# Kernel optimization log

Hardware: AMD Instinct MI355X
Metric: run time of the kernel (lower is better)

The kernel has to match this reference:

```python
import jax, jax.numpy as jnp
import numpy as np

B, L, E, H = 2, 2048, 1024, 16
D = E // H  # head dim = 64


def setup_inputs() -> dict:
    key = jax.random.key(0)
    ks = jax.random.split(key, 10)
    s = 0.02
    return {
        "xt": jax.random.normal(ks[0], (B, L, E), jnp.float32),
        "xs": jax.random.normal(ks[1], (B, L, E), jnp.float32),
        "Wt": jax.random.normal(ks[2], (E, 3 * E), jnp.float32) * s,  # t_attn weight (x @ Wt)
        "bt": jnp.zeros((3 * E,), jnp.float32),
        "Ws": jax.random.normal(ks[3], (E, 2 * E), jnp.float32) * s,  # s_attn weight
        "bs": jnp.zeros((2 * E,), jnp.float32),
        "Wc": jax.random.normal(ks[4], (E, E), jnp.float32) * s,      # c_proj weight
        "bc": jnp.zeros((E,), jnp.float32),
        "lam_ts": jnp.ones((1,), jnp.float32),
        "lam_st": jnp.ones((1,), jnp.float32),
        "lam_ss": jnp.ones((1,), jnp.float32),
    }


def _heads(x):
    # (B, L, E) -> (B, H, L, D)
    return x.reshape(B, L, H, D).transpose(0, 2, 1, 3)


def reference(xt, xs, Wt, bt, Ws, bs, Wc, bc, lam_ts, lam_st, lam_ss):
    qt, kt, vt = jnp.split(xt @ Wt + bt, 3, axis=2)
    qs, ks = jnp.split(xs @ Ws + bs, 2, axis=2)
    qt, kt, vt, qs, ks = map(_heads, (qt, kt, vt, qs, ks))

    # 4-way disentangled scores; fuse the 4 matmuls into 2 by combining keys:
    # qt@kt^T + lam_ts*qt@ks^T = qt @ (kt + lam_ts*ks)^T
    # lam_st*qs@kt^T + lam_ss*qs@ks^T = qs @ (lam_st*kt + lam_ss*ks)^T
    k1 = kt + lam_ts[0] * ks
    k2 = lam_st[0] * kt + lam_ss[0] * ks
    att = (jnp.einsum('bhqd,bhkd->bhqk', qt, k1)
           + jnp.einsum('bhqd,bhkd->bhqk', qs, k2)) * (1.0 / np.sqrt(D))
    att = jax.nn.softmax(att, axis=-1)
    y = jnp.einsum('bhqk,bhkd->bhqd', att, vt)  # (B, H, L, D)
    y = y.transpose(0, 2, 1, 3).reshape(B, L, E)
    return y @ Wc + bc
```

## Files before the change

kernel.cpp:

```cpp
#include <hip/hip_runtime.h>
#include <math.h>

#define LQ 2048
#define EQ 1024
#define M_ROWS 4096
#define BH 32

typedef _Float16 f16x8 __attribute__((ext_vector_type(8)));
typedef _Float16 f16x4 __attribute__((ext_vector_type(4)));
typedef _Float16 f16x2 __attribute__((ext_vector_type(2)));
typedef float f32x4 __attribute__((ext_vector_type(4)));
typedef float f32x16 __attribute__((ext_vector_type(16)));

#define QSCALE 0.1803368801111204f
#define DEFER_THR 8.0f

__device__ __forceinline__ void async_ld16(const _Float16* g, _Float16* l) {
  __builtin_amdgcn_global_load_lds(
      (const __attribute__((address_space(1))) unsigned int*)g,
      (__attribute__((address_space(3))) unsigned int*)l, 16, 0, 0);
}

__global__ __launch_bounds__(256) void prep(
    const float* __restrict__ xt, const float* __restrict__ xs,
    const float* __restrict__ Wt, const float* __restrict__ Ws,
    const float* __restrict__ Wc,
    _Float16* __restrict__ xt16, _Float16* __restrict__ xs16,
    _Float16* __restrict__ WtT, _Float16* __restrict__ WsT,
    _Float16* __restrict__ WcT) {
  int gb = blockIdx.x;
  if (gb < 4096) {
    int i = gb * 256 + threadIdx.x;
    const float* s; _Float16* d; size_t off;
    if (i < 524288) { s = xt; d = xt16; off = (size_t)i * 8; }
    else            { s = xs; d = xs16; off = (size_t)(i - 524288) * 8; }
    float4 a = *(const float4*)&s[off];
    float4 b = *(const float4*)&s[off + 4];
    f16x8 h;
    h[0] = (_Float16)a.x; h[1] = (_Float16)a.y; h[2] = (_Float16)a.z; h[3] = (_Float16)a.w;
    h[4] = (_Float16)b.x; h[5] = (_Float16)b.y; h[6] = (_Float16)b.z; h[7] = (_Float16)b.w;
    *(f16x8*)&d[off] = h;
  } else {
    __shared__ float T[32][65];
    int tb = gb - 4096;
    int c0 = (tb % 96) * 64;
    int k0 = (tb / 96) * 32;
    const float* W; _Float16* D; int Nw, cl;
    if (c0 < 3072)      { W = Wt; D = WtT; Nw = 3072; cl = c0; }
    else if (c0 < 5120) { W = Ws; D = WsT; Nw = 2048; cl = c0 - 3072; }
    else                { W = Wc; D = WcT; Nw = 1024; cl = c0 - 5120; }
    const int tid = threadIdx.x;
#pragma unroll
    for (int p = 0; p < 4; ++p) {
      int idx = tid + p * 256;
      int row = idx >> 5;
      int c2 = (idx & 31) * 2;
      float2 v = *(const float2*)&W[(size_t)(k0 + row) * Nw + cl + c2];
      T[row][c2] = v.x;
      T[row][c2 + 1] = v.y;
    }
    __syncthreads();
#pragma unroll
    for (int p = 0; p < 4; ++p) {
      int idx = tid + p * 256;
      int col = idx >> 4;
      int k2 = (idx & 15) * 2;
      f16x2 h2;
      h2[0] = (_Float16)T[k2][col];
      h2[1] = (_Float16)T[k2 + 1][col];
      *(f16x2*)&D[(size_t)(cl + col) * 1024 + k0 + k2] = h2;
    }
  }
}

__global__ __launch_bounds__(256, 3) void proj_gemm(
    const _Float16* __restrict__ xt16, const _Float16* __restrict__ xs16,
    const _Float16* __restrict__ WtT, const _Float16* __restrict__ WsT,
    const float* __restrict__ bt, const float* __restrict__ bs,
    _Float16* __restrict__ q16, _Float16* __restrict__ k16,
    _Float16* __restrict__ v16) {
  __shared__ _Float16 Al[128 * 64];
  __shared__ _Float16 Bl[128 * 64];

  const int tid = threadIdx.x;
  const int w = tid >> 6;
  const int lane = tid & 63;
  const int quad = lane >> 4;
  const int l15 = lane & 15;
  const int wm = w >> 1, wn = w & 1;
  const int by = blockIdx.y;
  const int n0 = blockIdx.x * 128;

  const _Float16* Ab;
  const _Float16* Bb;
  const float* bias;
  int m0, bsel = 0, branch;
  if (by < 32) {
    branch = 0; Ab = xt16; Bb = WtT; bias = bt; m0 = by * 128;
  } else if (by < 48) {
    branch = 1;
    int by2 = by - 32;
    bsel = by2 >> 3;
    m0 = (by2 & 7) * 128;
    Ab = WtT + (size_t)2048 * 1024;
    Bb = xt16 + (size_t)bsel * 2048 * 1024;
    bias = bt;
  } else {
    branch = 2; Ab = xs16; Bb = WsT; bias = bs; m0 = (by - 48) * 128;
  }

  const int srow = lane >> 3;
  const int sch = lane & 7;

  f32x4 acc[4][4];
#pragma unroll
  for (int mb = 0; mb < 4; ++mb)
#pragma unroll
    for (int nb = 0; nb < 4; ++nb) acc[mb][nb] = (f32x4){0.f, 0.f, 0.f, 0.f};

  for (int kt = 0; kt < 1024; kt += 64) {
    __syncthreads();
#pragma unroll
    for (int a = 0; a < 4; ++a) {
      int row = w * 32 + a * 8 + srow;
      int sc = sch ^ (row & 7);
      async_ld16(&Ab[(size_t)(m0 + row) * 1024 + kt + sc * 8], &Al[(w * 32 + a * 8) * 64]);
      async_ld16(&Bb[(size_t)(n0 + row) * 1024 + kt + sc * 8], &Bl[(w * 32 + a * 8) * 64]);
    }
    __syncthreads();

#pragma unroll
    for (int g = 0; g < 2; ++g) {
      f16x8 af[4], bf[4];
#pragma unroll
      for (int mb = 0; mb < 4; ++mb) {
        int row = wm * 64 + mb * 16 + l15;
        int pc = ((g * 4 + quad) ^ (row & 7)) * 8;
        af[mb] = *(const f16x8*)&Al[row * 64 + pc];
      }
#pragma unroll
      for (int nb = 0; nb < 4; ++nb) {
        int row = wn * 64 + nb * 16 + l15;
        int pc = ((g * 4 + quad) ^ (row & 7)) * 8;
        bf[nb] = *(const f16x8*)&Bl[row * 64 + pc];
      }
#pragma unroll
      for (int mb = 0; mb < 4; ++mb)
#pragma unroll
        for (int nb = 0; nb < 4; ++nb)
          acc[mb][nb] = __builtin_amdgcn_mfma_f32_16x16x32_f16(af[mb], bf[nb], acc[mb][nb], 0, 0, 0);
    }
  }

#pragma unroll
  for (int mb = 0; mb < 4; ++mb)
#pragma unroll
    for (int nb = 0; nb < 4; ++nb)
#pragma unroll
      for (int r = 0; r < 4; ++r) {
        int row = m0 + wm * 64 + mb * 16 + quad * 4 + r;
        int col = n0 + wn * 64 + nb * 16 + l15;
        if (branch == 1) {
          float val = acc[mb][nb][r] + bias[2048 + row];
          v16[(size_t)(bsel * 1024 + row) * 2048 + col] = (_Float16)val;
        } else {
          float val = acc[mb][nb][r] + bias[col];
          int bb = row >> 11, ll = row & 2047;
          int which = col >> 10, e = col & 1023;
          int hh = e >> 6, dd = e & 63;
          size_t rowhd = (size_t)(bb * 16 + hh) * 2048 + ll;
          int off = (branch == 0) ? 0 : 64;
          if (which == 0) q16[rowhd * 128 + off + dd] = (_Float16)val;
          else            k16[rowhd * 128 + off + dd] = (_Float16)val;
        }
      }
}

__global__ __launch_bounds__(256, 3) void cproj_gemm(
    const _Float16* __restrict__ A, const _Float16* __restrict__ Bm,
    const float* __restrict__ bias, float* __restrict__ outf) {
  __shared__ _Float16 Al0[128 * 32];
  __shared__ _Float16 Bl0[64 * 32];
  __shared__ _Float16 Al1[128 * 32];
  __shared__ _Float16 Bl1[64 * 32];

  const int tid = threadIdx.x;
  const int w = tid >> 6;
  const int lane = tid & 63;
  const int quad = lane >> 4;
  const int l15 = lane & 15;
  const int wm = w >> 1, wn = w & 1;
  const int m0 = blockIdx.y * 128;
  const int n0 = blockIdx.x * 64;

  const int srow = lane >> 2;
  const int schunk = ((lane & 3) ^ ((lane >> 3) & 3)) * 8;

  f32x4 acc[4][2];
#pragma unroll
  for (int mb = 0; mb < 4; ++mb)
#pragma unroll
    for (int nb = 0; nb < 2; ++nb) acc[mb][nb] = (f32x4){0.f, 0.f, 0.f, 0.f};

  const int key = (l15 >> 1) & 3;

  auto dma = [&](int kt, _Float16* Al, _Float16* Bl) {
#pragma unroll
    for (int i = 0; i < 2; ++i) {
      int rt = w * 32 + i * 16;
      async_ld16(&A[(size_t)(m0 + rt + srow) * 1024 + kt + schunk], &Al[rt * 32]);
    }
    int rtb = w * 16;
    async_ld16(&Bm[(size_t)(n0 + rtb + srow) * 1024 + kt + schunk], &Bl[rtb * 32]);
  };

  auto comp = [&](const _Float16* Al, const _Float16* Bl) {
    f16x8 af[4], bf[2];
    const int pc = (quad ^ key) * 8;
#pragma unroll
    for (int mb = 0; mb < 4; ++mb)
      af[mb] = *(const f16x8*)&Al[(wm * 64 + mb * 16 + l15) * 32 + pc];
#pragma unroll
    for (int nb = 0; nb < 2; ++nb)
      bf[nb] = *(const f16x8*)&Bl[(wn * 32 + nb * 16 + l15) * 32 + pc];
#pragma unroll
    for (int mb = 0; mb < 4; ++mb)
#pragma unroll
      for (int nb = 0; nb < 2; ++nb)
        acc[mb][nb] = __builtin_amdgcn_mfma_f32_16x16x32_f16(af[mb], bf[nb], acc[mb][nb], 0, 0, 0);
  };

  dma(0, Al0, Bl0);
  for (int kt = 0; kt < 1024; kt += 64) {
    __syncthreads();
    dma(kt + 32, Al1, Bl1);
    comp(Al0, Bl0);
    __syncthreads();
    if (kt + 64 < 1024) dma(kt + 64, Al0, Bl0);
    comp(Al1, Bl1);
  }

#pragma unroll
  for (int mb = 0; mb < 4; ++mb)
#pragma unroll
    for (int nb = 0; nb < 2; ++nb)
#pragma unroll
      for (int r = 0; r < 4; ++r) {
        int row = m0 + wm * 64 + mb * 16 + quad * 4 + r;
        int col = n0 + wn * 32 + nb * 16 + l15;
        outf[(size_t)row * 1024 + col] = acc[mb][nb][r] + bias[col];
      }
}

__global__ __launch_bounds__(256, 2) void flash_attn_mfma(
    const _Float16* __restrict__ qcat, const _Float16* __restrict__ kcat,
    const _Float16* __restrict__ vT, _Float16* __restrict__ y,
    const float* __restrict__ lam_ts, const float* __restrict__ lam_st,
    const float* __restrict__ lam_ss) {
  const int bh = blockIdx.y;
  const int qt0 = blockIdx.x * 128;
  const int b = bh >> 4, h = bh & 15;
  const _Float16* Qg = qcat + (size_t)bh * LQ * 128;
  const _Float16* Kg = kcat + (size_t)bh * LQ * 128;
  const _Float16* Vg = vT + (size_t)bh * 64 * LQ;

  __shared__ _Float16 Ksh0[64 * 128];
  __shared__ _Float16 Ksh1[64 * 128];
  __shared__ _Float16 Vsh0[64 * 64];
  __shared__ _Float16 Vsh1[64 * 64];
  __shared__ _Float16 Vsh2[64 * 64];
  __shared__ _Float16 Vsh3[64 * 64];

  const int tid = threadIdx.x;
  const int w = tid >> 6;
  const int lane = tid & 63;
  const int half = lane >> 5;
  const int l31 = lane & 31;

  const float lts = lam_ts[0], lst = lam_st[0], lss = lam_ss[0];

  f16x8 qf[8];
#pragma unroll
  for (int db = 0; db < 4; ++db) {
    const _Float16* qp = &Qg[(size_t)(qt0 + w * 32 + l31) * 128 + db * 16 + half * 8];
    f16x8 a = *(const f16x8*)qp;
    f16x8 bq = *(const f16x8*)(qp + 64);
#pragma unroll
    for (int e = 0; e < 8; ++e) {
      float fa = (float)a[e], fb = (float)bq[e];
      qf[db][e]     = (_Float16)(QSCALE * (fa + lst * fb));
      qf[db + 4][e] = (_Float16)(QSCALE * (lts * fa + lss * fb));
    }
  }

  float m_i = -INFINITY;
  float l_i = 0.f;
  f32x16 O[2];
#pragma unroll
  for (int nt = 0; nt < 2; ++nt)
#pragma unroll
    for (int r = 0; r < 16; ++r) O[nt][r] = 0.f;

  auto dma_k = [&](int t, _Float16* Kd) {
#pragma unroll
    for (int a = 0; a < 4; ++a) {
      int row = w * 16 + a * 4 + (lane >> 4);
      int sc = (lane & 15) ^ (row & 7);
      async_ld16(&Kg[(size_t)(t + row) * 128 + sc * 8], &Kd[(w * 16 + a * 4) * 128]);
    }
  };
  auto dma_v = [&](int t, _Float16* Vd) {
#pragma unroll
    for (int a = 0; a < 2; ++a) {
      int row = w * 16 + a * 8 + (lane >> 3);
      int sc = (lane & 7) ^ (row & 7);
      async_ld16(&Vg[(size_t)row * LQ + t + sc * 8], &Vd[(w * 16 + a * 8) * 64]);
    }
  };

  auto qk = [&](const _Float16* Ks, f32x16* Sp) {
    __builtin_amdgcn_s_setprio(1);
#pragma unroll
    for (int db = 0; db < 8; ++db) {
      const int pc = ((db * 2 + half) ^ (lane & 7)) * 8;
      f16x8 af0 = *(const f16x8*)&Ks[(l31) * 128 + pc];
      f16x8 af1 = *(const f16x8*)&Ks[(32 + l31) * 128 + pc];
      Sp[0] = __builtin_amdgcn_mfma_f32_32x32x16_f16(af0, qf[db], Sp[0], 0, 0, 0);
      Sp[1] = __builtin_amdgcn_mfma_f32_32x32x16_f16(af1, qf[db], Sp[1], 0, 0, 0);
    }
    __builtin_amdgcn_s_setprio(0);
  };

  auto softpv = [&](f32x16* S, const _Float16* Vs0, const _Float16* Vs1) {
    float mx = -INFINITY;
#pragma unroll
    for (int kb = 0; kb < 4; ++kb)
#pragma unroll
      for (int r = 0; r < 16; ++r) mx = fmaxf(mx, S[kb][r]);
    mx = fmaxf(mx, __shfl_xor(mx, 32));

    if (__any(mx > m_i + DEFER_THR)) {
      float m_new = fmaxf(m_i, mx);
      float alpha = __builtin_amdgcn_exp2f(m_i - m_new);
      l_i *= alpha;
#pragma unroll
      for (int nt = 0; nt < 2; ++nt)
#pragma unroll
        for (int r = 0; r < 16; ++r) O[nt][r] *= alpha;
      m_i = m_new;
    }

    float s = 0.f;
#pragma unroll
    for (int kb = 0; kb < 4; ++kb)
#pragma unroll
      for (int r = 0; r < 16; ++r) {
        float p = __builtin_amdgcn_exp2f(S[kb][r] - m_i);
        S[kb][r] = p;
        s += p;
      }
    s += __shfl_xor(s, 32);
    l_i += s;

#pragma unroll
    for (int kb = 0; kb < 4; ++kb) {
      unsigned pu[8];
#pragma unroll
      for (int i = 0; i < 8; ++i) {
        f16x2 t2;
        t2[0] = (_Float16)S[kb][2 * i];
        t2[1] = (_Float16)S[kb][2 * i + 1];
        pu[i] = __builtin_bit_cast(unsigned, t2);
      }
#pragma unroll
      for (int c = 0; c < 2; ++c) {
        unsigned u0 = pu[4 * c + 0], u1 = pu[4 * c + 1];
        unsigned u2 = pu[4 * c + 2], u3 = pu[4 * c + 3];
        asm("v_permlane32_swap_b32 %0, %1" : "+v"(u0), "+v"(u2));
        asm("v_permlane32_swap_b32 %0, %1" : "+v"(u1), "+v"(u3));
        union { unsigned u[4]; f16x8 v; } pb;
        pb.u[0] = u0; pb.u[1] = u1; pb.u[2] = u2; pb.u[3] = u3;
        const int kb2 = kb * 2 + c;
        const _Float16* Vs = (kb2 < 4) ? Vs0 : Vs1;
        const int kb2r = kb2 & 3;
        f16x8 av[2];
#pragma unroll
        for (int nt = 0; nt < 2; ++nt) {
          int dim = nt * 32 + l31;
          int pc = ((kb2r * 2 + half) ^ (dim & 7)) * 8;
          av[nt] = *(const f16x8*)&Vs[dim * 64 + pc];
        }
        __builtin_amdgcn_s_setprio(1);
#pragma unroll
        for (int nt = 0; nt < 2; ++nt)
          O[nt] = __builtin_amdgcn_mfma_f32_32x32x16_f16(av[nt], pb.v, O[nt], 0, 0, 0);
        __builtin_amdgcn_s_setprio(0);
      }
    }
  };

  auto step = [&](int t, const _Float16* Vr0, _Float16* Vr1, _Float16* Vw2) {
    f32x16 S[4];
#pragma unroll
    for (int kb = 0; kb < 4; ++kb)
#pragma unroll
      for (int r = 0; r < 16; ++r) S[kb][r] = 0.f;

    __syncthreads();
    dma_k(t + 64, Ksh1);
    dma_v(t + 64, Vr1);
    qk(Ksh0, &S[0]);
    __syncthreads();
    if (t + 128 < LQ) {
      dma_k(t + 128, Ksh0);
      dma_v(t + 128, Vw2);
    }
    qk(Ksh1, &S[2]);
    softpv(S, Vr0, Vr1);
  };

  dma_k(0, Ksh0);
  dma_v(0, Vsh0);
  for (int t = 0; t < LQ; t += 256) {
    step(t,       Vsh0, Vsh1, Vsh2);
    step(t + 128, Vsh2, Vsh3, Vsh0);
  }

  float inv = 1.f / l_i;
  int qrow = qt0 + w * 32 + l31;
#pragma unroll
  for (int nt = 0; nt < 2; ++nt)
#pragma unroll
    for (int rg = 0; rg < 4; ++rg) {
      f16x4 o4;
#pragma unroll
      for (int i = 0; i < 4; ++i) o4[i] = (_Float16)(O[nt][rg * 4 + i] * inv);
      int dim = nt * 32 + rg * 8 + half * 4;
      *(f16x4*)&y[((size_t)b * LQ + qrow) * EQ + h * 64 + dim] = o4;
    }
}

extern "C" void kernel_launch(void* const* d_in, const int* in_sizes, int n_in,
                              void* d_out, int out_size, void* d_ws, size_t ws_size,
                              hipStream_t stream) {
  const float* xt = (const float*)d_in[0];
  const float* xs = (const float*)d_in[1];
  const float* Wt = (const float*)d_in[2];
  const float* bt = (const float*)d_in[3];
  const float* Ws = (const float*)d_in[4];
  const float* bs = (const float*)d_in[5];
  const float* Wc = (const float*)d_in[6];
  const float* bc = (const float*)d_in[7];
  const float* lam_ts = (const float*)d_in[8];
  const float* lam_st = (const float*)d_in[9];
  const float* lam_ss = (const float*)d_in[10];
  float* out = (float*)d_out;

  _Float16* w16 = (_Float16*)d_ws;
  _Float16* xt16 = w16;
  _Float16* xs16 = xt16 + 4194304;
  _Float16* WtT  = xs16 + 4194304;
  _Float16* WsT  = WtT + 3145728;
  _Float16* WcT  = WsT + 2097152;
  _Float16* qcat = WcT + 1048576;
  _Float16* kcat = qcat + 8388608;
  _Float16* vbufT = kcat + 8388608;
  _Float16* ybuf = vbufT + 4194304;

  prep<<<7168, 256, 0, stream>>>(xt, xs, Wt, Ws, Wc, xt16, xs16, WtT, WsT, WcT);
  proj_gemm<<<dim3(16, 80), 256, 0, stream>>>(
      xt16, xs16, WtT, WsT, bt, bs, qcat, kcat, vbufT);
  flash_attn_mfma<<<dim3(16, 32), 256, 0, stream>>>(
      qcat, kcat, vbufT, ybuf, lam_ts, lam_st, lam_ss);
  cproj_gemm<<<dim3(16, 32), 256, 0, stream>>>(ybuf, WcT, bc, out);
}
```

Measured before the change: 258.1 us.

## Double-buffer projection GEMM and vectorize epilogue stores via swapped MFMA operands

```diff
diff --git a/kernel.cpp b/kernel.cpp
--- a/kernel.cpp
+++ b/kernel.cpp
@@ -79,8 +79,10 @@
     const float* __restrict__ bt, const float* __restrict__ bs,
     _Float16* __restrict__ q16, _Float16* __restrict__ k16,
     _Float16* __restrict__ v16) {
-  __shared__ _Float16 Al[128 * 64];
-  __shared__ _Float16 Bl[128 * 64];
+  __shared__ _Float16 Al0[128 * 32];
+  __shared__ _Float16 Bl0[128 * 32];
+  __shared__ _Float16 Al1[128 * 32];
+  __shared__ _Float16 Bl1[128 * 32];
 
   const int tid = threadIdx.x;
   const int w = tid >> 6;
@@ -109,8 +111,9 @@
     branch = 2; Ab = xs16; Bb = WsT; bias = bs; m0 = (by - 48) * 128;
   }
 
-  const int srow = lane >> 3;
-  const int sch = lane & 7;
+  const int srow = lane >> 2;
+  const int schunk = ((lane & 3) ^ ((lane >> 3) & 3)) * 8;
+  const int key = (l15 >> 1) & 3;
 
   f32x4 acc[4][4];
 #pragma unroll
@@ -118,62 +121,71 @@
 #pragma unroll
     for (int nb = 0; nb < 4; ++nb) acc[mb][nb] = (f32x4){0.f, 0.f, 0.f, 0.f};
 
+  auto dma = [&](int kt, _Float16* Al, _Float16* Bl) {
+#pragma unroll
+    for (int i = 0; i < 2; ++i) {
+      int rt = w * 32 + i * 16;
+      async_ld16(&Ab[(size_t)(m0 + rt + srow) * 1024 + kt + schunk], &Al[rt * 32]);
+      async_ld16(&Bb[(size_t)(n0 + rt + srow) * 1024 + kt + schunk], &Bl[rt * 32]);
+    }
+  };
+
+  auto comp = [&](const _Float16* Al, const _Float16* Bl) {
+    f16x8 af[4], bf[4];
+    const int pc = (quad ^ key) * 8;
+#pragma unroll
+    for (int mb = 0; mb < 4; ++mb)
+      af[mb] = *(const f16x8*)&Al[(wm * 64 + mb * 16 + l15) * 32 + pc];
+#pragma unroll
+    for (int nb = 0; nb < 4; ++nb)
+      bf[nb] = *(const f16x8*)&Bl[(wn * 64 + nb * 16 + l15) * 32 + pc];
+#pragma unroll
+    for (int mb = 0; mb < 4; ++mb)
+#pragma unroll
+      for (int nb = 0; nb < 4; ++nb)
+        acc[mb][nb] = __builtin_amdgcn_mfma_f32_16x16x32_f16(bf[nb], af[mb], acc[mb][nb], 0, 0, 0);
+  };
+
+  dma(0, Al0, Bl0);
   for (int kt = 0; kt < 1024; kt += 64) {
     __syncthreads();
-#pragma unroll
-    for (int a = 0; a < 4; ++a) {
-      int row = w * 32 + a * 8 + srow;
-      int sc = sch ^ (row & 7);
-      async_ld16(&Ab[(size_t)(m0 + row) * 1024 + kt + sc * 8], &Al[(w * 32 + a * 8) * 64]);
-      async_ld16(&Bb[(size_t)(n0 + row) * 1024 + kt + sc * 8], &Bl[(w * 32 + a * 8) * 64]);
-    }
-    __syncthreads();
-
-#pragma unroll
-    for (int g = 0; g < 2; ++g) {
-      f16x8 af[4], bf[4];
-#pragma unroll
-      for (int mb = 0; mb < 4; ++mb) {
-        int row = wm * 64 + mb * 16 + l15;
-        int pc = ((g * 4 + quad) ^ (row & 7)) * 8;
-        af[mb] = *(const f16x8*)&Al[row * 64 + pc];
+    dma(kt + 32, Al1, Bl1);
+    comp(Al0, Bl0);
+    __syncthreads();
+    if (kt + 64 < 1024) dma(kt + 64, Al0, Bl0);
+    comp(Al1, Bl1);
+  }
+
+#pragma unroll
+  for (int nb = 0; nb < 4; ++nb) {
+    const int col0 = n0 + wn * 64 + nb * 16 + quad * 4;
+    float4 bv4;
+    if (branch != 1) bv4 = *(const float4*)&bias[col0];
+#pragma unroll
+    for (int mb = 0; mb < 4; ++mb) {
+      int row = m0 + wm * 64 + mb * 16 + l15;
+      if (branch == 1) {
+        float bv = bias[2048 + row];
+        f16x4 o4;
+#pragma unroll
+        for (int r = 0; r < 4; ++r) o4[r] = (_Float16)(acc[mb][nb][r] + bv);
+        *(f16x4*)&v16[(size_t)(bsel * 1024 + row) * 2048 + col0] = o4;
+      } else {
+        f16x4 o4;
+        o4[0] = (_Float16)(acc[mb][nb][0] + bv4.x);
+        o4[1] = (_Float16)(acc[mb][nb][1] + bv4.y);
+        o4[2] = (_Float16)(acc[mb][nb][2] + bv4.z);
+        o4[3] = (_Float16)(acc[mb][nb][3] + bv4.w);
+        int bb = row >> 11, ll = row & 2047;
+        int which = col0 >> 10, e = col0 & 1023;
+        int hh = e >> 6, dd = e & 63;
+        size_t rowhd = (size_t)(bb * 16 + hh) * 2048 + ll;
+        int off = (branch == 0) ? 0 : 64;
+        _Float16* dst = (which == 0) ? q16 : k16;
+        *(f16x4*)&dst[rowhd * 128 + off + dd] = o4;
       }
-#pragma unroll
-      for (int nb = 0; nb < 4; ++nb) {
-        int row = wn * 64 + nb * 16 + l15;
-        int pc = ((g * 4 + quad) ^ (row & 7)) * 8;
-        bf[nb] = *(const f16x8*)&Bl[row * 64 + pc];
-      }
-#pragma unroll
-      for (int mb = 0; mb < 4; ++mb)
-#pragma unroll
-        for (int nb = 0; nb < 4; ++nb)
-          acc[mb][nb] = __builtin_amdgcn_mfma_f32_16x16x32_f16(af[mb], bf[nb], acc[mb][nb], 0, 0, 0);
-    }
-  }
-
-#pragma unroll
-  for (int mb = 0; mb < 4; ++mb)
-#pragma unroll
-    for (int nb = 0; nb < 4; ++nb)
-#pragma unroll
-      for (int r = 0; r < 4; ++r) {
-        int row = m0 + wm * 64 + mb * 16 + quad * 4 + r;
-        int col = n0 + wn * 64 + nb * 16 + l15;
-        if (branch == 1) {
-          float val = acc[mb][nb][r] + bias[2048 + row];
-          v16[(size_t)(bsel * 1024 + row) * 2048 + col] = (_Float16)val;
-        } else {
-          float val = acc[mb][nb][r] + bias[col];
-          int bb = row >> 11, ll = row & 2047;
-          int which = col >> 10, e = col & 1023;
-          int hh = e >> 6, dd = e & 63;
-          size_t rowhd = (size_t)(bb * 16 + hh) * 2048 + ll;
-          int off = (branch == 0) ? 0 : 64;
-          if (which == 0) q16[rowhd * 128 + off + dd] = (_Float16)val;
-          else            k16[rowhd * 128 + off + dd] = (_Float16)val;
-        }
-      }
+    }
+  }
 }
 
 __global__ __launch_bounds__(256, 3) void cproj_gemm(
@@ -227,7 +239,7 @@
     for (int mb = 0; mb < 4; ++mb)
 #pragma unroll
       for (int nb = 0; nb < 2; ++nb)
-        acc[mb][nb] = __builtin_amdgcn_mfma_f32_16x16x32_f16(af[mb], bf[nb], acc[mb][nb], 0, 0, 0);
+        acc[mb][nb] = __builtin_amdgcn_mfma_f32_16x16x32_f16(bf[nb], af[mb], acc[mb][nb], 0, 0, 0);
   };
 
   dma(0, Al0, Bl0);
@@ -241,15 +253,20 @@
   }
 
 #pragma unroll
-  for (int mb = 0; mb < 4; ++mb)
-#pragma unroll
-    for (int nb = 0; nb < 2; ++nb)
-#pragma unroll
-      for (int r = 0; r < 4; ++r) {
-        int row = m0 + wm * 64 + mb * 16 + quad * 4 + r;
-        int col = n0 + wn * 32 + nb * 16 + l15;
-        outf[(size_t)row * 1024 + col] = acc[mb][nb][r] + bias[col];
-      }
+  for (int nb = 0; nb < 2; ++nb) {
+    const int col0 = n0 + wn * 32 + nb * 16 + quad * 4;
+    const float4 bv4 = *(const float4*)&bias[col0];
+#pragma unroll
+    for (int mb = 0; mb < 4; ++mb) {
+      int row = m0 + wm * 64 + mb * 16 + l15;
+      float4 o4;
+      o4.x = acc[mb][nb][0] + bv4.x;
+      o4.y = acc[mb][nb][1] + bv4.y;
+      o4.z = acc[mb][nb][2] + bv4.z;
+      o4.w = acc[mb][nb][3] + bv4.w;
+      *(float4*)&outf[(size_t)row * 1024 + col0] = o4;
+    }
+  }
 }
 
 __global__ __launch_bounds__(256, 2) void flash_attn_mfma(
```

Result: slower. 266.0 us (+3.1%).
